# Kernel optimization log

Measured on AMD Instinct MI355X. Metric: run time of the kernel, lower is better.

Reference implementation:

```python
import jax, jax.numpy as jnp
import numpy as np

NEG_SLOPE = 0.2
LN_EPS = 1e-5


def setup_inputs() -> dict:
    key = jax.random.key(0)
    k1, k2, k3, k4 = jax.random.split(key, 4)
    B, K, D, H = 64, 256, 1024, 2
    x = jax.random.normal(k1, (B, K, D), dtype=jnp.float32)
    adj = jax.random.randint(k2, (K, K), 0, 2, dtype=jnp.int32)
    # Xavier-ish scaling for weights
    W = jax.random.normal(k3, (D, D), dtype=jnp.float32) * (1.0 / np.sqrt(D))
    a = jax.random.normal(k4, (H, 2 * D), dtype=jnp.float32) * (1.0 / np.sqrt(2 * D))
    gamma = jnp.ones((D,), dtype=jnp.float32)
    beta = jnp.zeros((D,), dtype=jnp.float32)
    return {"x": x, "adj": adj, "W": W, "a": a, "gamma": gamma, "beta": beta}


def _layer_norm(y, gamma, beta):
    mu = jnp.mean(y, axis=-1, keepdims=True)
    var = jnp.mean(jnp.square(y - mu), axis=-1, keepdims=True)
    return (y - mu) * jax.lax.rsqrt(var + LN_EPS) * gamma + beta


def reference(x, adj, W, a, gamma, beta):
    # x: (B,K,D), adj: (K,K), W: (D,D), a: (H,2D)
    D = W.shape[1]
    h = jnp.einsum("bki,io->bko", x, W)  # (B,K,D)
    # GAT trick: a^T [h_i; h_j] = a_src . h_i + a_dst . h_j (same math as
    # the huge pairwise-concat + Linear in the original module).
    a_src, a_dst = a[:, :D], a[:, D:]  # each (H,D)
    f_i = jnp.einsum("bkd,hd->bhk", h, a_src)  # (B,H,K)
    f_j = jnp.einsum("bkd,hd->bhk", h, a_dst)  # (B,H,K)
    e = f_i[:, :, :, None] + f_j[:, :, None, :]  # (B,H,K,K)
    e = jnp.where(e >= 0, e, NEG_SLOPE * e)  # LeakyReLU
    mask = (adj != 0)[None, None]  # (1,1,K,K)
    e = jnp.where(mask, e, -jnp.inf)
    attn = jax.nn.softmax(e, axis=-1)
    attn = jnp.where(jnp.isnan(attn), 0.0, attn)  # nan_to_num for all-masked rows
    # dropout is identity in eval mode
    head_out = jnp.einsum("bhij,bjd->bhid", attn, h)  # (B,H,K,D)
    out = jnp.mean(head_out, axis=1)  # average heads, (B,K,D)
    out = _layer_norm(out + x, gamma, beta)  # residual is Identity (in_dim==out_dim)
    return out
```

## Files before the change

### kernel.cpp

```cpp
#include <hip/hip_runtime.h>
#include <hip/hip_bf16.h>

#define KN 256
#define DD 1024
#define HH 2

typedef __attribute__((ext_vector_type(8))) short short8;
typedef __attribute__((ext_vector_type(4))) float f32x4;

__device__ __forceinline__ ushort f2b(float f) {
  union { float f; unsigned u; } v; v.f = f;
  unsigned u = v.u;
  return (ushort)((u + 0x7fffu + ((u >> 16) & 1u)) >> 16);
}
__device__ __forceinline__ float b2f(ushort h) {
  union { unsigned u; float f; } v; v.u = ((unsigned)h) << 16;
  return v.f;
}
__device__ __forceinline__ void gload16(const ushort* g, ushort* l) {
  __builtin_amdgcn_global_load_lds(
      (const __attribute__((address_space(1))) void*)g,
      (__attribute__((address_space(3))) void*)l, 16, 0, 0);
}

__global__ __launch_bounds__(256) void k_conv(const float* __restrict__ x,
                                              ushort* __restrict__ xb) {
  int c0 = blockIdx.x * 256 + threadIdx.x;
  for (int it = 0; it < 4; ++it) {
    size_t i = ((size_t)c0 + (size_t)it * 524288) * 8;
    float4 v0 = *reinterpret_cast<const float4*>(&x[i]);
    float4 v1 = *reinterpret_cast<const float4*>(&x[i + 4]);
    short8 o;
    o[0] = (short)f2b(v0.x); o[1] = (short)f2b(v0.y);
    o[2] = (short)f2b(v0.z); o[3] = (short)f2b(v0.w);
    o[4] = (short)f2b(v1.x); o[5] = (short)f2b(v1.y);
    o[6] = (short)f2b(v1.z); o[7] = (short)f2b(v1.w);
    *reinterpret_cast<short8*>(&xb[i]) = o;
  }
}

__global__ __launch_bounds__(256) void k_wT(const float* __restrict__ W, ushort* __restrict__ WTb) {
  __shared__ float t[32][33];
  int tx = threadIdx.x, ty = threadIdx.y;
  int x = blockIdx.x * 32 + tx;
  int y0 = blockIdx.y * 32 + ty;
  for (int i = 0; i < 32; i += 8)
    t[ty + i][tx] = W[(size_t)(y0 + i) * DD + x];
  __syncthreads();
  int xo = blockIdx.y * 32 + tx;
  int yo = blockIdx.x * 32 + ty;
  for (int i = 0; i < 32; i += 8)
    WTb[(size_t)(yo + i) * DD + xo] = f2b(t[tx][ty + i]);
}

__device__ __forceinline__ void gh_stage(const ushort* gA0, const ushort* gB0, int kt,
                                         ushort* As, ushort* Bs, int tid) {
  int wb = tid & ~63;
  #pragma unroll
  for (int s = 0; s < 2; ++s) {
    int c = s * 512 + tid;
    int row = c >> 2, kc = c & 3;
    gload16(gA0 + (size_t)row * DD + kt + kc * 8, As + (size_t)(s * 512 + wb) * 8);
    gload16(gB0 + (size_t)row * DD + kt + kc * 8, Bs + (size_t)(s * 512 + wb) * 8);
  }
}

__global__ __launch_bounds__(512, 2) void k_gemm_h(const ushort* __restrict__ xb,
                                                   const ushort* __restrict__ WTb,
                                                   ushort* __restrict__ hT) {
  __shared__ ushort As[2][8192];
  __shared__ ushort Bs[2][8192];
  const int tid = threadIdx.x;
  const int b = blockIdx.x;
  const int bn = blockIdx.y;
  const int w = tid >> 6, lane = tid & 63;
  const int wm = (w >> 2) * 128, wn = (w & 3) * 64;
  const int r16 = lane & 15, kqi = lane >> 4;
  const ushort* gA0 = xb + (size_t)(b * 256) * DD;
  const ushort* gB0 = WTb + (size_t)(bn * 256) * DD;
  f32x4 acc[8][4] = {};

  gh_stage(gA0, gB0, 0, As[0], Bs[0], tid);
  gh_stage(gA0, gB0, 32, As[1], Bs[1], tid);
  for (int it = 0; it < 32; ++it) {
    const int cur = it & 1;
    if (it < 31) asm volatile("s_waitcnt vmcnt(4)" ::: "memory");
    else         asm volatile("s_waitcnt vmcnt(0)" ::: "memory");
    __builtin_amdgcn_s_barrier();
    __builtin_amdgcn_sched_barrier(0);
    const ushort* Ac = As[cur];
    const ushort* Bc = Bs[cur];
    short8 af[8], bf[4];
    #pragma unroll
    for (int mf = 0; mf < 8; ++mf) {
      int row = wm + mf * 16 + r16;
      af[mf] = *reinterpret_cast<const short8*>(Ac + (size_t)row * 32 + kqi * 8);
    }
    #pragma unroll
    for (int nf = 0; nf < 4; ++nf) {
      int row = wn + nf * 16 + r16;
      bf[nf] = *reinterpret_cast<const short8*>(Bc + (size_t)row * 32 + kqi * 8);
    }
    #pragma unroll
    for (int mf = 0; mf < 8; ++mf)
      #pragma unroll
      for (int nf = 0; nf < 4; ++nf)
        acc[mf][nf] = __builtin_amdgcn_mfma_f32_16x16x32_bf16(af[mf], bf[nf], acc[mf][nf], 0, 0, 0);
    __builtin_amdgcn_sched_barrier(0);
    __builtin_amdgcn_s_barrier();
    if (it < 30)
      gh_stage(gA0, gB0, (it + 2) * 32, As[cur], Bs[cur], tid);
  }
  const int g = lane >> 4;
  #pragma unroll
  for (int mf = 0; mf < 8; ++mf) {
    int j0 = wm + mf * 16 + g * 4;
    #pragma unroll
    for (int nf = 0; nf < 4; ++nf) {
      int C = bn * 256 + wn + nf * 16 + r16;
      ushort4 o;
      o.x = f2b(acc[mf][nf][0]); o.y = f2b(acc[mf][nf][1]);
      o.z = f2b(acc[mf][nf][2]); o.w = f2b(acc[mf][nf][3]);
      *reinterpret_cast<ushort4*>(&hT[((size_t)b * DD + C) * KN + j0]) = o;
    }
  }
}

__global__ __launch_bounds__(256) void k_f(const ushort* __restrict__ hT,
                                           const float* __restrict__ a,
                                           float* __restrict__ fip, float* __restrict__ fjp) {
  __shared__ float als[4][256];
  int b = blockIdx.x, dq = blockIdx.y;
  int tid = threadIdx.x;
  for (int v = 0; v < 4; ++v) als[v][tid] = a[v * DD + dq * 256 + tid];
  __syncthreads();
  const ushort* base = hT + ((size_t)b * DD + dq * 256) * KN + tid;
  float a0 = 0.f, a1 = 0.f, a2 = 0.f, a3 = 0.f;
  #pragma unroll 8
  for (int d = 0; d < 256; ++d) {
    float hv = b2f(base[(size_t)d * KN]);
    a0 += hv * als[0][d];
    a1 += hv * als[1][d];
    a2 += hv * als[2][d];
    a3 += hv * als[3][d];
  }
  size_t o = ((size_t)(dq * 64 + b) * HH) * KN + tid;
  fip[o] = a0;
  fjp[o] = a1;
  fip[o + KN] = a2;
  fjp[o + KN] = a3;
}

__global__ __launch_bounds__(256) void k_attn(const float* __restrict__ fip, const float* __restrict__ fjp,
                                              const int* __restrict__ adj, ushort* __restrict__ Pb) {
  int w = threadIdx.x >> 6, l = threadIdx.x & 63;
  int gw = blockIdx.x * 4 + w;
  int b = gw >> 8, i = gw & 255;
  int4 am = *reinterpret_cast<const int4*>(adj + i * KN + l * 4);
  int msk[4] = { am.x, am.y, am.z, am.w };
  float fi0 = 0.f, fi1 = 0.f;
  float fj0[4] = {0.f, 0.f, 0.f, 0.f}, fj1[4] = {0.f, 0.f, 0.f, 0.f};
  for (int dq = 0; dq < 4; ++dq) {
    size_t o = ((size_t)(dq * 64 + b) * HH) * KN;
    fi0 += fip[o + i];
    fi1 += fip[o + KN + i];
    float4 t0 = *reinterpret_cast<const float4*>(&fjp[o + l * 4]);
    float4 t1 = *reinterpret_cast<const float4*>(&fjp[o + KN + l * 4]);
    fj0[0] += t0.x; fj0[1] += t0.y; fj0[2] += t0.z; fj0[3] += t0.w;
    fj1[0] += t1.x; fj1[1] += t1.y; fj1[2] += t1.z; fj1[3] += t1.w;
  }
  float e0[4], e1[4];
  const float NEGINF = -3.0e38f;
  float m0 = NEGINF, m1 = NEGINF;
  for (int e = 0; e < 4; ++e) {
    float v0 = fi0 + fj0[e], v1 = fi1 + fj1[e];
    v0 = v0 >= 0.f ? v0 : 0.2f * v0;
    v1 = v1 >= 0.f ? v1 : 0.2f * v1;
    e0[e] = v0; e1[e] = v1;
    if (msk[e]) { m0 = fmaxf(m0, v0); m1 = fmaxf(m1, v1); }
  }
  for (int off = 1; off < 64; off <<= 1) {
    m0 = fmaxf(m0, __shfl_xor(m0, off));
    m1 = fmaxf(m1, __shfl_xor(m1, off));
  }
  float p0[4], p1[4], s0 = 0.f, s1 = 0.f;
  for (int e = 0; e < 4; ++e) {
    p0[e] = msk[e] ? __expf(e0[e] - m0) : 0.f;
    p1[e] = msk[e] ? __expf(e1[e] - m1) : 0.f;
    s0 += p0[e]; s1 += p1[e];
  }
  for (int off = 1; off < 64; off <<= 1) {
    s0 += __shfl_xor(s0, off);
    s1 += __shfl_xor(s1, off);
  }
  float i0 = s0 > 0.f ? 1.f / s0 : 0.f;
  float i1 = s1 > 0.f ? 1.f / s1 : 0.f;
  ushort4 o;
  o.x = f2b(0.5f * (p0[0] * i0 + p1[0] * i1));
  o.y = f2b(0.5f * (p0[1] * i0 + p1[1] * i1));
  o.z = f2b(0.5f * (p0[2] * i0 + p1[2] * i1));
  o.w = f2b(0.5f * (p0[3] * i0 + p1[3] * i1));
  *reinterpret_cast<ushort4*>(&Pb[((size_t)b * KN + i) * KN + l * 4]) = o;
}

__global__ __launch_bounds__(512) void k_gemm_o(const ushort* __restrict__ Pb,
                                                const ushort* __restrict__ hT,
                                                const float* __restrict__ x,
                                                const ushort* __restrict__ xb,
                                                int use_xb,
                                                ushort* __restrict__ y,
                                                float* __restrict__ pstats) {
  __shared__ ushort As[2][8192];
  __shared__ ushort Bs[2][4096];
  __shared__ float red2[256][2][2];
  const int b = blockIdx.x;
  const int dt = blockIdx.y;
  const int tid = threadIdx.x;
  const int w = tid >> 6, lane = tid & 63;
  const int wm = (w >> 1) * 64;
  const int wn = (w & 1) * 64;
  const int r16 = lane & 15, kqi = lane >> 4;
  const ushort* PbB = Pb + (size_t)b * KN * KN;
  const ushort* hTB = hT + ((size_t)b * DD + dt * 128) * KN;
  f32x4 acc[4][4] = {};
  const int wb = tid & ~63;

  #define OSTAGE(buf, kt)                                                          \
    {                                                                              \
      _Pragma("unroll")                                                            \
      for (int s = 0; s < 2; ++s) {                                                \
        int slot = s * 512 + tid;                                                  \
        int row = slot >> 2, kc = slot & 3;                                        \
        gload16(PbB + (size_t)row * KN + (kt) + kc * 8,                            \
                As[buf] + (size_t)(s * 512 + wb) * 8);                             \
      }                                                                            \
      {                                                                            \
        int row = tid >> 2, kc = tid & 3;                                          \
        gload16(hTB + (size_t)row * KN + (kt) + kc * 8,                            \
                Bs[buf] + (size_t)wb * 8);                                         \
      }                                                                            \
    }

  OSTAGE(0, 0);
  OSTAGE(1, 32);
  for (int it8 = 0; it8 < 8; ++it8) {
    const int cur = it8 & 1;
    if (it8 < 7) asm volatile("s_waitcnt vmcnt(3)" ::: "memory");
    else         asm volatile("s_waitcnt vmcnt(0)" ::: "memory");
    __builtin_amdgcn_s_barrier();
    __builtin_amdgcn_sched_barrier(0);
    const ushort* Ac = As[cur];
    const ushort* Bc = Bs[cur];
    short8 af[4], bf[4];
    #pragma unroll
    for (int mf = 0; mf < 4; ++mf) {
      int row = wm + mf * 16 + r16;
      af[mf] = *reinterpret_cast<const short8*>(Ac + (size_t)row * 32 + kqi * 8);
    }
    #pragma unroll
    for (int nf = 0; nf < 4; ++nf) {
      int row = wn + nf * 16 + r16;
      bf[nf] = *reinterpret_cast<const short8*>(Bc + (size_t)row * 32 + kqi * 8);
    }
    #pragma unroll
    for (int mf = 0; mf < 4; ++mf)
      #pragma unroll
      for (int nf = 0; nf < 4; ++nf)
        acc[mf][nf] = __builtin_amdgcn_mfma_f32_16x16x32_bf16(af[mf], bf[nf], acc[mf][nf], 0, 0, 0);
    __builtin_amdgcn_sched_barrier(0);
    __builtin_amdgcn_s_barrier();
    if (it8 < 6)
      OSTAGE(cur, (it8 + 2) * 32);
  }
  #undef OSTAGE

  const int g = lane >> 4;
  float ps[4][4] = {}, qs[4][4] = {};
  #pragma unroll
  for (int mf = 0; mf < 4; ++mf)
    #pragma unroll
    for (int nf = 0; nf < 4; ++nf) {
      int C = dt * 128 + wn + nf * 16 + r16;
      #pragma unroll
      for (int rr = 0; rr < 4; ++rr) {
        int i = wm + mf * 16 + g * 4 + rr;
        size_t gi = ((size_t)(b * KN + i)) * DD + C;
        float rv = use_xb ? b2f(xb[gi]) : x[gi];
        float v = acc[mf][nf][rr] + rv;
        y[gi] = f2b(v);
        ps[mf][rr] += v; qs[mf][rr] += v * v;
      }
    }
  #pragma unroll
  for (int off = 1; off < 16; off <<= 1)
    #pragma unroll
    for (int mf = 0; mf < 4; ++mf)
      #pragma unroll
      for (int rr = 0; rr < 4; ++rr) {
        ps[mf][rr] += __shfl_xor(ps[mf][rr], off);
        qs[mf][rr] += __shfl_xor(qs[mf][rr], off);
      }
  if (r16 == 0) {
    #pragma unroll
    for (int mf = 0; mf < 4; ++mf)
      #pragma unroll
      for (int rr = 0; rr < 4; ++rr) {
        int i = wm + mf * 16 + g * 4 + rr;
        red2[i][w & 1][0] = ps[mf][rr];
        red2[i][w & 1][1] = qs[mf][rr];
      }
  }
  __syncthreads();
  if (tid < 256) {
    float S = red2[tid][0][0] + red2[tid][1][0];
    float Q = red2[tid][0][1] + red2[tid][1][1];
    size_t o = ((size_t)(dt * 64 + b) * KN + tid) * 2;
    pstats[o] = S;
    pstats[o + 1] = Q;
  }
}

__global__ __launch_bounds__(256) void k_ln(const ushort* __restrict__ y,
                                            const float* __restrict__ pstats,
                                            const float* __restrict__ gamma,
                                            const float* __restrict__ beta,
                                            float* __restrict__ out) {
  int tid = threadIdx.x;
  size_t row = blockIdx.x;
  int b = (int)(row >> 8), i = (int)(row & 255);
  float S = 0.f, Q = 0.f;
  #pragma unroll
  for (int dt = 0; dt < 8; ++dt) {
    size_t o = ((size_t)(dt * 64 + b) * KN + i) * 2;
    S += pstats[o];
    Q += pstats[o + 1];
  }
  float mu = S * (1.0f / DD);
  float var = Q * (1.0f / DD) - mu * mu;
  float inv = rsqrtf(var + 1e-5f);
  ushort4 v = *reinterpret_cast<const ushort4*>(&y[row * DD + tid * 4]);
  float4 gm = *reinterpret_cast<const float4*>(&gamma[tid * 4]);
  float4 bt = *reinterpret_cast<const float4*>(&beta[tid * 4]);
  float4 o;
  o.x = (b2f(v.x) - mu) * inv * gm.x + bt.x;
  o.y = (b2f(v.y) - mu) * inv * gm.y + bt.y;
  o.z = (b2f(v.z) - mu) * inv * gm.z + bt.z;
  o.w = (b2f(v.w) - mu) * inv * gm.w + bt.w;
  *reinterpret_cast<float4*>(&out[row * DD + tid * 4]) = o;
}

extern "C" void kernel_launch(void* const* d_in, const int* in_sizes, int n_in,
                              void* d_out, int out_size, void* d_ws, size_t ws_size,
                              hipStream_t stream) {
  const float* x     = (const float*)d_in[0];
  const int*   adj   = (const int*)d_in[1];
  const float* W     = (const float*)d_in[2];
  const float* a     = (const float*)d_in[3];
  const float* gamma = (const float*)d_in[4];
  const float* beta  = (const float*)d_in[5];
  float* out = (float*)d_out;

  char* ws = (char*)d_ws;
  const size_t OFS_WT = 0;
  const size_t OFS_XB = 2097152;
  const size_t OFS_HT = 35651584;
  const size_t OFS_PB = 69206016;
  const size_t NEED     = 77856768;
  const size_t NEED_BIG = 111411200;
  if (ws_size < NEED) return;
  const int use_xb = (ws_size >= NEED_BIG) ? 1 : 0;

  ushort* WTb   = (ushort*)(ws + OFS_WT);
  float*  fip   = (float*)(ws + OFS_WT);
  float*  fjp   = (float*)(ws + OFS_WT + 524288);
  float*  pst   = (float*)(ws + OFS_WT);
  ushort* xb    = (ushort*)(ws + OFS_XB);
  ushort* hT    = (ushort*)(ws + OFS_HT);
  ushort* Pb    = (ushort*)(ws + OFS_PB);
  ushort* y     = use_xb ? (ushort*)(ws + NEED) : (ushort*)(ws + OFS_XB);

  k_conv<<<2048, 256, 0, stream>>>(x, xb);
  k_wT<<<dim3(32, 32), dim3(32, 8), 0, stream>>>(W, WTb);
  k_gemm_h<<<dim3(64, 4), 512, 0, stream>>>(xb, WTb, hT);
  k_f<<<dim3(64, 4), 256, 0, stream>>>(hT, a, fip, fjp);
  k_attn<<<4096, 256, 0, stream>>>(fip, fjp, adj, Pb);
  k_gemm_o<<<dim3(64, 8), 512, 0, stream>>>(Pb, hT, x, xb, use_xb, y, pst);
  k_ln<<<16384, 256, 0, stream>>>(y, pst, gamma, beta, out);
}
```

Baseline: 145.6 us.

## Rework h GEMM pipeline with BK=64 swizzled LDS and phased prefetch; residual in place

The h GEMM moves from a 32-wide K tile with a double buffer to a 64-wide K tile. The LDS layout gets an XOR swizzle to avoid bank conflicts, and the schedule is split into eight phases that interleave global-to-LDS staging with MFMA work. It also raises wave priority around the MFMA bursts and swaps the grid order so blocks sharing a weight tile run together. The output GEMM now reads the bf16 residual from the xb buffer and writes the sum back in place. This drops the fp32 x read path and the separate y buffer, at the cost of using a bf16 residual and doubling LDS per block, which may limit occupancy.

```diff
diff --git a/kernel.cpp b/kernel.cpp
--- a/kernel.cpp
+++ b/kernel.cpp
@@ -53,64 +53,104 @@
     WTb[(size_t)(yo + i) * DD + xo] = f2b(t[tx][ty + i]);
 }
 
-__device__ __forceinline__ void gh_stage(const ushort* gA0, const ushort* gB0, int kt,
-                                         ushort* As, ushort* Bs, int tid) {
-  int wb = tid & ~63;
-  #pragma unroll
-  for (int s = 0; s < 2; ++s) {
-    int c = s * 512 + tid;
-    int row = c >> 2, kc = c & 3;
-    gload16(gA0 + (size_t)row * DD + kt + kc * 8, As + (size_t)(s * 512 + wb) * 8);
-    gload16(gB0 + (size_t)row * DD + kt + kc * 8, Bs + (size_t)(s * 512 + wb) * 8);
-  }
-}
-
 __global__ __launch_bounds__(512, 2) void k_gemm_h(const ushort* __restrict__ xb,
                                                    const ushort* __restrict__ WTb,
                                                    ushort* __restrict__ hT) {
-  __shared__ ushort As[2][8192];
-  __shared__ ushort Bs[2][8192];
+  __shared__ ushort As[2][16384];
+  __shared__ ushort Bs[2][16384];
   const int tid = threadIdx.x;
-  const int b = blockIdx.x;
-  const int bn = blockIdx.y;
   const int w = tid >> 6, lane = tid & 63;
+  const int bn = blockIdx.x;
+  const int b  = blockIdx.y;
   const int wm = (w >> 2) * 128, wn = (w & 3) * 64;
   const int r16 = lane & 15, kqi = lane >> 4;
   const ushort* gA0 = xb + (size_t)(b * 256) * DD;
   const ushort* gB0 = WTb + (size_t)(bn * 256) * DD;
+  const int srow0 = tid >> 3;
+  const int scc   = (tid & 7) ^ ((tid >> 3) & 7);
+  const int sdst0 = (tid & ~63) * 8;
+  const int cs0 = (kqi)     ^ (r16 & 7);
+  const int cs1 = (kqi + 4) ^ (r16 & 7);
   f32x4 acc[8][4] = {};
-
-  gh_stage(gA0, gB0, 0, As[0], Bs[0], tid);
-  gh_stage(gA0, gB0, 32, As[1], Bs[1], tid);
-  for (int it = 0; it < 32; ++it) {
-    const int cur = it & 1;
-    if (it < 31) asm volatile("s_waitcnt vmcnt(4)" ::: "memory");
-    else         asm volatile("s_waitcnt vmcnt(0)" ::: "memory");
-    __builtin_amdgcn_s_barrier();
-    __builtin_amdgcn_sched_barrier(0);
-    const ushort* Ac = As[cur];
-    const ushort* Bc = Bs[cur];
-    short8 af[8], bf[4];
-    #pragma unroll
-    for (int mf = 0; mf < 8; ++mf) {
-      int row = wm + mf * 16 + r16;
-      af[mf] = *reinterpret_cast<const short8*>(Ac + (size_t)row * 32 + kqi * 8);
-    }
-    #pragma unroll
-    for (int nf = 0; nf < 4; ++nf) {
-      int row = wn + nf * 16 + r16;
-      bf[nf] = *reinterpret_cast<const short8*>(Bc + (size_t)row * 32 + kqi * 8);
-    }
-    #pragma unroll
-    for (int mf = 0; mf < 8; ++mf)
-      #pragma unroll
-      for (int nf = 0; nf < 4; ++nf)
-        acc[mf][nf] = __builtin_amdgcn_mfma_f32_16x16x32_bf16(af[mf], bf[nf], acc[mf][nf], 0, 0, 0);
-    __builtin_amdgcn_sched_barrier(0);
-    __builtin_amdgcn_s_barrier();
-    if (it < 30)
-      gh_stage(gA0, gB0, (it + 2) * 32, As[cur], Bs[cur], tid);
-  }
+  short8 bfv[4][2];
+
+#define STG(ISB, BUF, H, KB)                                                    \
+  {                                                                             \
+    const ushort* g0_ = (ISB) ? gB0 : gA0;                                      \
+    ushort* l0_ = (ISB) ? Bs[BUF] : As[BUF];                                    \
+    gload16(g0_ + (size_t)((H) * 128 + srow0) * DD + (KB) + scc * 8,            \
+            l0_ + (H) * 8192 + sdst0);                                          \
+    gload16(g0_ + (size_t)((H) * 128 + 64 + srow0) * DD + (KB) + scc * 8,       \
+            l0_ + (H) * 8192 + 4096 + sdst0);                                   \
+  }
+
+#define PHASE(Q, BUF, LOADB, WMODE, STAGE_STMT)                                 \
+  {                                                                             \
+    short8 af0[2], af1[2];                                                      \
+    {                                                                           \
+      const ushort* Ab_ = As[BUF];                                              \
+      int ra_ = (wm + (Q) * 32 + r16) * 64;                                     \
+      int rb_ = (wm + (Q) * 32 + 16 + r16) * 64;                                \
+      af0[0] = *(const short8*)(Ab_ + ra_ + cs0 * 8);                           \
+      af0[1] = *(const short8*)(Ab_ + ra_ + cs1 * 8);                           \
+      af1[0] = *(const short8*)(Ab_ + rb_ + cs0 * 8);                           \
+      af1[1] = *(const short8*)(Ab_ + rb_ + cs1 * 8);                           \
+    }                                                                           \
+    if (LOADB) {                                                                \
+      const ushort* Bb_ = Bs[BUF];                                              \
+      _Pragma("unroll")                                                         \
+      for (int nf = 0; nf < 4; ++nf) {                                          \
+        int rn_ = (wn + nf * 16 + r16) * 64;                                    \
+        bfv[nf][0] = *(const short8*)(Bb_ + rn_ + cs0 * 8);                     \
+        bfv[nf][1] = *(const short8*)(Bb_ + rn_ + cs1 * 8);                     \
+      }                                                                         \
+    }                                                                           \
+    STAGE_STMT;                                                                 \
+    __builtin_amdgcn_s_barrier();                                               \
+    asm volatile("s_waitcnt lgkmcnt(0)" ::: "memory");                          \
+    __builtin_amdgcn_sched_barrier(0);                                          \
+    __builtin_amdgcn_s_setprio(1);                                              \
+    _Pragma("unroll")                                                           \
+    for (int nf = 0; nf < 4; ++nf) {                                            \
+      acc[(Q)*2][nf]   = __builtin_amdgcn_mfma_f32_16x16x32_bf16(af0[0], bfv[nf][0], acc[(Q)*2][nf], 0, 0, 0);     \
+      acc[(Q)*2+1][nf] = __builtin_amdgcn_mfma_f32_16x16x32_bf16(af1[0], bfv[nf][0], acc[(Q)*2+1][nf], 0, 0, 0);   \
+    }                                                                           \
+    _Pragma("unroll")                                                           \
+    for (int nf = 0; nf < 4; ++nf) {                                            \
+      acc[(Q)*2][nf]   = __builtin_amdgcn_mfma_f32_16x16x32_bf16(af0[1], bfv[nf][1], acc[(Q)*2][nf], 0, 0, 0);     \
+      acc[(Q)*2+1][nf] = __builtin_amdgcn_mfma_f32_16x16x32_bf16(af1[1], bfv[nf][1], acc[(Q)*2+1][nf], 0, 0, 0);   \
+    }                                                                           \
+    __builtin_amdgcn_s_setprio(0);                                              \
+    __builtin_amdgcn_sched_barrier(0);                                          \
+    if ((WMODE) == 1) { asm volatile("s_waitcnt vmcnt(6)" ::: "memory"); }      \
+    else if ((WMODE) == 2) { asm volatile("s_waitcnt vmcnt(0)" ::: "memory"); } \
+    __builtin_amdgcn_s_barrier();                                               \
+  }
+
+  STG(1, 0, 0, 0) STG(1, 0, 1, 0) STG(0, 0, 0, 0) STG(0, 0, 1, 0)
+  STG(1, 1, 0, 64) STG(1, 1, 1, 64) STG(0, 1, 0, 64)
+  asm volatile("s_waitcnt vmcnt(6)" ::: "memory");
+  __builtin_amdgcn_sched_barrier(0);
+  __builtin_amdgcn_s_barrier();
+
+  for (int i = 0; i < 8; ++i) {
+    const int k1 = i * 128 + 64;
+    const int k2 = i * 128 + 128;
+    const int k3 = i * 128 + 192;
+    const bool s2 = (k2 < 1024), s3 = (k3 < 1024);
+    const int wt = (i < 7) ? 1 : 2;
+    PHASE(0, 0, 1, 0,  { STG(0, 1, 1, k1) })
+    PHASE(1, 0, 0, 0,  { if (s2) STG(1, 0, 0, k2) })
+    PHASE(2, 0, 0, 0,  { if (s2) STG(1, 0, 1, k2) })
+    PHASE(3, 0, 0, wt, { if (s2) STG(0, 0, 0, k2) })
+    PHASE(0, 1, 1, 0,  { if (s2) STG(0, 0, 1, k2) })
+    PHASE(1, 1, 0, 0,  { if (s3) STG(1, 1, 0, k3) })
+    PHASE(2, 1, 0, 0,  { if (s3) STG(1, 1, 1, k3) })
+    PHASE(3, 1, 0, wt, { if (s3) STG(0, 1, 0, k3) })
+  }
+#undef PHASE
+#undef STG
+
   const int g = lane >> 4;
   #pragma unroll
   for (int mf = 0; mf < 8; ++mf) {
@@ -205,10 +245,7 @@
 
 __global__ __launch_bounds__(512) void k_gemm_o(const ushort* __restrict__ Pb,
                                                 const ushort* __restrict__ hT,
-                                                const float* __restrict__ x,
-                                                const ushort* __restrict__ xb,
-                                                int use_xb,
-                                                ushort* __restrict__ y,
+                                                ushort* __restrict__ yx,
                                                 float* __restrict__ pstats) {
   __shared__ ushort As[2][8192];
   __shared__ ushort Bs[2][4096];
@@ -285,9 +322,8 @@
       for (int rr = 0; rr < 4; ++rr) {
         int i = wm + mf * 16 + g * 4 + rr;
         size_t gi = ((size_t)(b * KN + i)) * DD + C;
-        float rv = use_xb ? b2f(xb[gi]) : x[gi];
-        float v = acc[mf][nf][rr] + rv;
-        y[gi] = f2b(v);
+        float v = acc[mf][nf][rr] + b2f(yx[gi]);
+        yx[gi] = f2b(v);
         ps[mf][rr] += v; qs[mf][rr] += v * v;
       }
     }
@@ -365,10 +401,8 @@
   const size_t OFS_XB = 2097152;
   const size_t OFS_HT = 35651584;
   const size_t OFS_PB = 69206016;
-  const size_t NEED     = 77856768;
-  const size_t NEED_BIG = 111411200;
+  const size_t NEED   = 77856768;
   if (ws_size < NEED) return;
-  const int use_xb = (ws_size >= NEED_BIG) ? 1 : 0;
 
   ushort* WTb   = (ushort*)(ws + OFS_WT);
   float*  fip   = (float*)(ws + OFS_WT);
@@ -377,13 +411,12 @@
   ushort* xb    = (ushort*)(ws + OFS_XB);
   ushort* hT    = (ushort*)(ws + OFS_HT);
   ushort* Pb    = (ushort*)(ws + OFS_PB);
-  ushort* y     = use_xb ? (ushort*)(ws + NEED) : (ushort*)(ws + OFS_XB);
 
   k_conv<<<2048, 256, 0, stream>>>(x, xb);
   k_wT<<<dim3(32, 32), dim3(32, 8), 0, stream>>>(W, WTb);
-  k_gemm_h<<<dim3(64, 4), 512, 0, stream>>>(xb, WTb, hT);
+  k_gemm_h<<<dim3(4, 64), 512, 0, stream>>>(xb, WTb, hT);
   k_f<<<dim3(64, 4), 256, 0, stream>>>(hT, a, fip, fjp);
   k_attn<<<4096, 256, 0, stream>>>(fip, fjp, adj, Pb);
-  k_gemm_o<<<dim3(64, 8), 512, 0, stream>>>(Pb, hT, x, xb, use_xb, y, pst);
-  k_ln<<<16384, 256, 0, stream>>>(y, pst, gamma, beta, out);
-}
+  k_gemm_o<<<dim3(64, 8), 512, 0, stream>>>(Pb, hT, xb, pst);
+  k_ln<<<16384, 256, 0, stream>>>(xb, pst, gamma, beta, out);
+}
```

Result: faster. 137.5 us (-5.6%).
